# Kernel optimization log

Measured on AMD Instinct MI355X. Metric: run time of the kernel, lower is better.

## Reference

```python
import jax, jax.numpy as jnp
import numpy as np

B, T, C, H, W = 4, 8, 128, 96, 96
D = 64  # d_model

def setup_inputs() -> dict:
    key = jax.random.key(0)
    ks = jax.random.split(key, 7)
    return {
        "x": jax.random.normal(ks[0], (B, T, C, H, W), dtype=jnp.float32),
        "Wq": jax.random.normal(ks[1], (D, C), dtype=jnp.float32) * (1.0 / np.sqrt(C)),
        "bq": jax.random.normal(ks[2], (D,), dtype=jnp.float32) * 0.01,
        "Wk": jax.random.normal(ks[3], (D, C), dtype=jnp.float32) * (1.0 / np.sqrt(C)),
        "bk": jax.random.normal(ks[4], (D,), dtype=jnp.float32) * 0.01,
        "Wv": jax.random.normal(ks[5], (C, C), dtype=jnp.float32) * (1.0 / np.sqrt(C)),
        "bv": jax.random.normal(ks[6], (C,), dtype=jnp.float32) * 0.01,
    }

def reference(x, Wq, bq, Wk, bk, Wv, bv):
    # x: (B, T, C, H, W). 1x1 convs == per-pixel channel matmuls.
    d_model = Wq.shape[0]
    scale = 1.0 / jnp.sqrt(jnp.asarray(d_model, x.dtype))
    # Project and land directly in (B, H, W, T, feat) layout (fuses the permutes).
    Q = jnp.einsum('btchw,dc->bhwtd', x, Wq) + bq  # (B,H,W,T,D)
    K = jnp.einsum('btchw,dc->bhwtd', x, Wk) + bk  # (B,H,W,T,D)
    V = jnp.einsum('btchw,ec->bhwte', x, Wv) + bv  # (B,H,W,T,C)
    scores = jnp.einsum('bhwtd,bhwsd->bhwts', Q, K) * scale  # (B,H,W,T,T)
    attn = jax.nn.softmax(scores, axis=-1)
    out = jnp.einsum('bhwts,bhwse->bhwte', attn, V)  # (B,H,W,T,C)
    return jnp.transpose(out, (0, 3, 4, 1, 2))  # (B,T,C,H,W)
```

## Files before the change

### kernel.cpp

```cpp
#include <hip/hip_runtime.h>
#include <hip/hip_bf16.h>

#define TT 8
#define CC 128
#define DD 64
#define HWp 9216
#define PP 16
#define XB_STRIDE 152
#define QKV_STRIDE 264

typedef __attribute__((ext_vector_type(8))) short short8;
typedef __attribute__((ext_vector_type(4))) short short4v;
typedef __attribute__((ext_vector_type(4))) float floatx4;

__device__ __forceinline__ short f2bf(float f) {
    __hip_bfloat16 h = __float2bfloat16(f);
    return __builtin_bit_cast(short, h);
}
__device__ __forceinline__ float bf2f(short s) {
    unsigned u = ((unsigned)(unsigned short)s) << 16;
    return __builtin_bit_cast(float, u);
}

__global__ __launch_bounds__(512, 4) void ta_kernel(
    const float* __restrict__ x,
    const float* __restrict__ Wq, const float* __restrict__ bq,
    const float* __restrict__ Wk, const float* __restrict__ bk,
    const float* __restrict__ Wv, const float* __restrict__ bv,
    float* __restrict__ out)
{
    __shared__ short xb[PP * XB_STRIDE];
    __shared__ short qkv[TT * PP * QKV_STRIDE];

    const int tid  = threadIdx.x;
    const int wave = tid >> 6;
    const int lane = tid & 63;
    const int quad = lane >> 4;
    const int l16  = lane & 15;

    const int blk = blockIdx.x;
    const int b   = blk / (HWp / PP);
    const int p0  = (blk % (HWp / PP)) * PP;

    short8 wfrag[2][4];
    float  bias[2][4];
#pragma unroll
    for (int i = 0; i < 2; ++i) {
        const int f0  = (wave * 2 + i) * 16;
        const int row = f0 + l16;
        const float* wrow;
        if (row < DD)            wrow = Wq + row * CC;
        else if (row < 2 * DD)   wrow = Wk + (row - DD) * CC;
        else                     wrow = Wv + (row - 2 * DD) * CC;
#pragma unroll
        for (int kc = 0; kc < 4; ++kc) {
            const float* src = wrow + kc * 32 + quad * 8;
            short8 v;
#pragma unroll
            for (int j = 0; j < 8; ++j) v[j] = f2bf(src[j]);
            wfrag[i][kc] = v;
        }
        const int fb = f0 + quad * 4;
        const float* bsrc; int off;
        if (fb < DD)            { bsrc = bq; off = fb; }
        else if (fb < 2 * DD)   { bsrc = bk; off = fb - DD; }
        else                    { bsrc = bv; off = fb - 2 * DD; }
#pragma unroll
        for (int r = 0; r < 4; ++r) bias[i][r] = bsrc[off + r];
    }

    const int c0 = tid >> 2;
    const int p4 = (tid & 3) * 4;
    const float* xsrc0 = x + ((size_t)(b * TT) * CC + c0) * HWp + p0 + p4;

    float4 cur = *(const float4*)xsrc0;
    for (int t = 0; t < TT; ++t) {
        float4 nxt = cur;
        if (t < TT - 1)
            nxt = *(const float4*)(xsrc0 + (size_t)(t + 1) * CC * HWp);

        __syncthreads();
        xb[(p4 + 0) * XB_STRIDE + c0] = f2bf(cur.x);
        xb[(p4 + 1) * XB_STRIDE + c0] = f2bf(cur.y);
        xb[(p4 + 2) * XB_STRIDE + c0] = f2bf(cur.z);
        xb[(p4 + 3) * XB_STRIDE + c0] = f2bf(cur.w);
        __syncthreads();

        floatx4 acc[2];
#pragma unroll
        for (int i = 0; i < 2; ++i)
#pragma unroll
            for (int r = 0; r < 4; ++r) acc[i][r] = 0.f;
#pragma unroll
        for (int kc = 0; kc < 4; ++kc) {
            short8 xf = *(const short8*)&xb[l16 * XB_STRIDE + kc * 32 + quad * 8];
            acc[0] = __builtin_amdgcn_mfma_f32_16x16x32_bf16(wfrag[0][kc], xf, acc[0], 0, 0, 0);
            acc[1] = __builtin_amdgcn_mfma_f32_16x16x32_bf16(wfrag[1][kc], xf, acc[1], 0, 0, 0);
        }
#pragma unroll
        for (int i = 0; i < 2; ++i) {
            const int f0 = (wave * 2 + i) * 16 + quad * 4;
            short4v o;
#pragma unroll
            for (int r = 0; r < 4; ++r) o[r] = f2bf(acc[i][r] + bias[i][r]);
            *(short4v*)&qkv[(t * PP + l16) * QKV_STRIDE + f0] = o;
        }
        cur = nxt;
    }
    __syncthreads();

    {
        const int p  = tid & 15;
        const int g  = tid >> 4;
        const int tq = g >> 2;
        const int e0 = (g & 3) * 32;

        const short* qrow = &qkv[(tq * PP + p) * QKV_STRIDE];
        float qv[DD];
#pragma unroll
        for (int dc = 0; dc < 8; ++dc) {
            short8 v = *(const short8*)(qrow + dc * 8);
#pragma unroll
            for (int j = 0; j < 8; ++j) qv[dc * 8 + j] = bf2f(v[j]);
        }
        float sc[TT];
#pragma unroll
        for (int s = 0; s < TT; ++s) {
            const short* krow = &qkv[(s * PP + p) * QKV_STRIDE + DD];
            float a = 0.f;
#pragma unroll
            for (int dc = 0; dc < 8; ++dc) {
                short8 v = *(const short8*)(krow + dc * 8);
#pragma unroll
                for (int j = 0; j < 8; ++j) a += qv[dc * 8 + j] * bf2f(v[j]);
            }
            sc[s] = a * 0.125f;
        }
        float m = sc[0];
#pragma unroll
        for (int s = 1; s < TT; ++s) m = fmaxf(m, sc[s]);
        float sum = 0.f;
#pragma unroll
        for (int s = 0; s < TT; ++s) { sc[s] = __expf(sc[s] - m); sum += sc[s]; }
        const float inv = 1.f / sum;
#pragma unroll
        for (int s = 0; s < TT; ++s) sc[s] *= inv;

        float o[32];
#pragma unroll
        for (int j = 0; j < 32; ++j) o[j] = 0.f;
#pragma unroll
        for (int s = 0; s < TT; ++s) {
            const short* vrow = &qkv[(s * PP + p) * QKV_STRIDE + 2 * DD + e0];
            const float a = sc[s];
#pragma unroll
            for (int ec = 0; ec < 4; ++ec) {
                short8 v = *(const short8*)(vrow + ec * 8);
#pragma unroll
                for (int j = 0; j < 8; ++j) o[ec * 8 + j] += a * bf2f(v[j]);
            }
        }
        float* op = out + ((size_t)((b * TT + tq) * CC + e0)) * HWp + p0 + p;
#pragma unroll
        for (int e = 0; e < 32; ++e) op[(size_t)e * HWp] = o[e];
    }
}

extern "C" void kernel_launch(void* const* d_in, const int* in_sizes, int n_in,
                              void* d_out, int out_size, void* d_ws, size_t ws_size,
                              hipStream_t stream) {
    const float* x  = (const float*)d_in[0];
    const float* Wq = (const float*)d_in[1];
    const float* bq = (const float*)d_in[2];
    const float* Wk = (const float*)d_in[3];
    const float* bk = (const float*)d_in[4];
    const float* Wv = (const float*)d_in[5];
    const float* bv = (const float*)d_in[6];
    float* out = (float*)d_out;

    const int blocks = 4 * (HWp / PP);
    ta_kernel<<<blocks, 512, 0, stream>>>(x, Wq, bq, Wk, bk, Wv, bv, out);
}
```

Baseline: 340.1 us.

## Halve pixel tile, pack two timesteps per MFMA pass, split attention dot across lanes

Each block now covers 8 pixels instead of 16. Two timesteps are stacked into one 16-row MFMA projection pass, so the loop runs 4 iterations instead of 8. The attention stage splits the QK dot product across 8 lanes with shuffle reductions, which cuts per-thread register use (64-float q vector, 32 outputs). Launch bounds now target 8 blocks per CU and block IDs are remapped to interleave tiles, aiming for higher occupancy and better memory-level parallelism. In exchange, the weight fragments are reloaded twice as often and global accesses are narrower (32 B pixel runs), which may hurt coalescing.

```diff
diff --git a/kernel.cpp b/kernel.cpp
--- a/kernel.cpp
+++ b/kernel.cpp
@@ -5,7 +5,8 @@
 #define CC 128
 #define DD 64
 #define HWp 9216
-#define PP 16
+#define PP 8
+#define NTILE 1152
 #define XB_STRIDE 152
 #define QKV_STRIDE 264
 
@@ -22,14 +23,14 @@
     return __builtin_bit_cast(float, u);
 }
 
-__global__ __launch_bounds__(512, 4) void ta_kernel(
+__global__ __launch_bounds__(512, 8) void ta_kernel(
     const float* __restrict__ x,
     const float* __restrict__ Wq, const float* __restrict__ bq,
     const float* __restrict__ Wk, const float* __restrict__ bk,
     const float* __restrict__ Wv, const float* __restrict__ bv,
     float* __restrict__ out)
 {
-    __shared__ short xb[PP * XB_STRIDE];
+    __shared__ short xb[16 * XB_STRIDE];
     __shared__ short qkv[TT * PP * QKV_STRIDE];
 
     const int tid  = threadIdx.x;
@@ -38,9 +39,10 @@
     const int quad = lane >> 4;
     const int l16  = lane & 15;
 
-    const int blk = blockIdx.x;
-    const int b   = blk / (HWp / PP);
-    const int p0  = (blk % (HWp / PP)) * PP;
+    const int orig = blockIdx.x;
+    const int L    = (orig & 7) * (4 * NTILE / 8) + (orig >> 3);
+    const int b    = L / NTILE;
+    const int p0   = (L % NTILE) * PP;
 
     short8 wfrag[2][4];
     float  bias[2][4];
@@ -69,21 +71,23 @@
         for (int r = 0; r < 4; ++r) bias[i][r] = bsrc[off + r];
     }
 
-    const int c0 = tid >> 2;
-    const int p4 = (tid & 3) * 4;
-    const float* xsrc0 = x + ((size_t)(b * TT) * CC + c0) * HWp + p0 + p4;
+    const int c0   = tid >> 2;
+    const int toff = (tid >> 1) & 1;
+    const int p4   = (tid & 1) * 4;
+    const float* xsrc0 = x + ((size_t)(b * TT + toff) * CC + c0) * HWp + p0 + p4;
 
     float4 cur = *(const float4*)xsrc0;
-    for (int t = 0; t < TT; ++t) {
+    for (int tp = 0; tp < 4; ++tp) {
         float4 nxt = cur;
-        if (t < TT - 1)
-            nxt = *(const float4*)(xsrc0 + (size_t)(t + 1) * CC * HWp);
+        if (tp < 3)
+            nxt = *(const float4*)(xsrc0 + (size_t)(tp + 1) * 2 * CC * HWp);
 
         __syncthreads();
-        xb[(p4 + 0) * XB_STRIDE + c0] = f2bf(cur.x);
-        xb[(p4 + 1) * XB_STRIDE + c0] = f2bf(cur.y);
-        xb[(p4 + 2) * XB_STRIDE + c0] = f2bf(cur.z);
-        xb[(p4 + 3) * XB_STRIDE + c0] = f2bf(cur.w);
+        const int xrow = toff * PP + p4;
+        xb[(xrow + 0) * XB_STRIDE + c0] = f2bf(cur.x);
+        xb[(xrow + 1) * XB_STRIDE + c0] = f2bf(cur.y);
+        xb[(xrow + 2) * XB_STRIDE + c0] = f2bf(cur.z);
+        xb[(xrow + 3) * XB_STRIDE + c0] = f2bf(cur.w);
         __syncthreads();
 
         floatx4 acc[2];
@@ -103,66 +107,70 @@
             short4v o;
 #pragma unroll
             for (int r = 0; r < 4; ++r) o[r] = f2bf(acc[i][r] + bias[i][r]);
-            *(short4v*)&qkv[(t * PP + l16) * QKV_STRIDE + f0] = o;
+            *(short4v*)&qkv[(tp * 16 + l16) * QKV_STRIDE + f0] = o;
         }
         cur = nxt;
     }
     __syncthreads();
 
     {
-        const int p  = tid & 15;
-        const int g  = tid >> 4;
-        const int tq = g >> 2;
-        const int e0 = (g & 3) * 32;
+        const int p   = tid & 7;
+        const int dsl = (tid >> 3) & 7;
+        const int tq  = wave;
 
-        const short* qrow = &qkv[(tq * PP + p) * QKV_STRIDE];
-        float qv[DD];
+        const short* prow = &qkv[p * QKV_STRIDE];
+
+        float qv[8];
+        {
+            short8 v = *(const short8*)(prow + (tq * PP) * QKV_STRIDE + dsl * 8);
 #pragma unroll
-        for (int dc = 0; dc < 8; ++dc) {
-            short8 v = *(const short8*)(qrow + dc * 8);
-#pragma unroll
-            for (int j = 0; j < 8; ++j) qv[dc * 8 + j] = bf2f(v[j]);
+            for (int j = 0; j < 8; ++j) qv[j] = bf2f(v[j]);
         }
         float sc[TT];
 #pragma unroll
         for (int s = 0; s < TT; ++s) {
-            const short* krow = &qkv[(s * PP + p) * QKV_STRIDE + DD];
+            short8 v = *(const short8*)(prow + (s * PP) * QKV_STRIDE + DD + dsl * 8);
             float a = 0.f;
 #pragma unroll
-            for (int dc = 0; dc < 8; ++dc) {
-                short8 v = *(const short8*)(krow + dc * 8);
+            for (int j = 0; j < 8; ++j) a = fmaf(qv[j], bf2f(v[j]), a);
+            sc[s] = a;
+        }
 #pragma unroll
-                for (int j = 0; j < 8; ++j) a += qv[dc * 8 + j] * bf2f(v[j]);
-            }
-            sc[s] = a * 0.125f;
-        }
-        float m = sc[0];
+        for (int m = 8; m <= 32; m <<= 1)
 #pragma unroll
-        for (int s = 1; s < TT; ++s) m = fmaxf(m, sc[s]);
+            for (int s = 0; s < TT; ++s) sc[s] += __shfl_xor(sc[s], m, 64);
+
+        float mx = sc[0];
+#pragma unroll
+        for (int s = 1; s < TT; ++s) mx = fmaxf(mx, sc[s]);
         float sum = 0.f;
 #pragma unroll
-        for (int s = 0; s < TT; ++s) { sc[s] = __expf(sc[s] - m); sum += sc[s]; }
+        for (int s = 0; s < TT; ++s) {
+            float e = __expf((sc[s] - mx) * 0.125f);
+            sc[s] = e; sum += e;
+        }
         const float inv = 1.f / sum;
 #pragma unroll
         for (int s = 0; s < TT; ++s) sc[s] *= inv;
 
-        float o[32];
+        float o[16];
 #pragma unroll
-        for (int j = 0; j < 32; ++j) o[j] = 0.f;
+        for (int j = 0; j < 16; ++j) o[j] = 0.f;
 #pragma unroll
         for (int s = 0; s < TT; ++s) {
-            const short* vrow = &qkv[(s * PP + p) * QKV_STRIDE + 2 * DD + e0];
+            const short* vr = prow + (s * PP) * QKV_STRIDE + 2 * DD + dsl * 16;
+            short8 v0 = *(const short8*)vr;
+            short8 v1 = *(const short8*)(vr + 8);
             const float a = sc[s];
 #pragma unroll
-            for (int ec = 0; ec < 4; ++ec) {
-                short8 v = *(const short8*)(vrow + ec * 8);
-#pragma unroll
-                for (int j = 0; j < 8; ++j) o[ec * 8 + j] += a * bf2f(v[j]);
+            for (int j = 0; j < 8; ++j) {
+                o[j]     = fmaf(a, bf2f(v0[j]), o[j]);
+                o[8 + j] = fmaf(a, bf2f(v1[j]), o[8 + j]);
             }
         }
-        float* op = out + ((size_t)((b * TT + tq) * CC + e0)) * HWp + p0 + p;
+        float* op = out + ((size_t)((b * TT + tq) * CC + dsl * 16)) * HWp + p0 + p;
 #pragma unroll
-        for (int e = 0; e < 32; ++e) op[(size_t)e * HWp] = o[e];
+        for (int e = 0; e < 16; ++e) op[(size_t)e * HWp] = o[e];
     }
 }
 
@@ -178,6 +186,6 @@
     const float* bv = (const float*)d_in[6];
     float* out = (float*)d_out;
 
-    const int blocks = 4 * (HWp / PP);
+    const int blocks = 4 * NTILE;
     ta_kernel<<<blocks, 512, 0, stream>>>(x, Wq, bq, Wk, bk, Wv, bv, out);
 }
```

After: 408.3 us. 1.2x slower.
